# Optimization experiments

Hardware: AMD Instinct MI355X
Metric: run time of the kernel (lower is better)

## Reference

```python
import jax, jax.numpy as jnp
import numpy as np

N = 100000          # number of nodes (nums)
E = 1200000         # nnz of the normalized adjacency
D = 64              # embed_size; layer_size = [64, 64, 64]
NODE_DROP = 0.1     # args.node_dropout[0]
MESS_DROP = (0.1, 0.1, 0.1)
EPS = 1e-12         # F.normalize eps


def setup_inputs() -> dict:
    key = jax.random.key(0)
    ks = jax.random.split(key, 10)
    rows = jax.random.randint(ks[0], (E,), 0, N, dtype=jnp.int32)
    cols = jax.random.randint(ks[1], (E,), 0, N, dtype=jnp.int32)
    vals = jax.random.uniform(ks[2], (E,), dtype=jnp.float32)
    emb = jax.random.normal(ks[3], (N, D), dtype=jnp.float32) * 0.1
    W0 = jax.random.normal(ks[4], (D, D), dtype=jnp.float32) * 0.1
    b0 = jax.random.normal(ks[5], (1, D), dtype=jnp.float32) * 0.1
    W1 = jax.random.normal(ks[6], (D, D), dtype=jnp.float32) * 0.1
    b1 = jax.random.normal(ks[7], (1, D), dtype=jnp.float32) * 0.1
    W2 = jax.random.normal(ks[8], (D, D), dtype=jnp.float32) * 0.1
    b2 = jax.random.normal(ks[9], (1, D), dtype=jnp.float32) * 0.1
    return dict(rows=rows, cols=cols, vals=vals, emb=emb,
                W0=W0, b0=b0, W1=W1, b1=b1, W2=W2, b2=b2)


def reference(rows, cols, vals, emb, W0, b0, W1, b1, W2, b2):
    drop_key = jax.random.key(42)
    k_node, k0, k1, k2 = jax.random.split(drop_key, 4)

    # sparse node dropout: zero dropped edge values (== removing nnz), scale survivors
    keep_e = jax.random.bernoulli(k_node, 1.0 - NODE_DROP, (E,))
    a_vals = jnp.where(keep_e, vals / (1.0 - NODE_DROP), 0.0)

    def layer(ego, W, b, rate, k):
        # SpMM: out[r] += a_vals * ego[c]   (COO scatter-add)
        side = jax.ops.segment_sum(a_vals[:, None] * ego[cols], rows, num_segments=N)
        h = side @ W + b
        keep = jax.random.bernoulli(k, 1.0 - rate, h.shape)
        h = jnp.where(keep, h / (1.0 - rate), 0.0)          # mess dropout
        nrm = h / jnp.maximum(jnp.linalg.norm(h, axis=1, keepdims=True), EPS)
        return h, nrm  # ego continues as the (un-normalized) dropped output

    all_embs = [emb]
    ego = emb
    for (W, b, rate, k) in ((W0, b0, MESS_DROP[0], k0),
                            (W1, b1, MESS_DROP[1], k1),
                            (W2, b2, MESS_DROP[2], k2)):
        ego, nrm = layer(ego, W, b, rate, k)
        all_embs.append(nrm)
    return jnp.concatenate(all_embs, axis=1)  # [N, 4*D]
```

## Files before the change

kernel.cpp:

```cpp
#include <hip/hip_runtime.h>
#include <stdint.h>

#define N_NODES 100000
#define DIM 64
#define E_EDGES 1200000
#define NBK 6250
#define NREP 8
#define BCAP_R 64
#define ROW_CAP 40
#define BPB 16

__host__ __device__ __forceinline__ void tf2x32(uint32_t k0, uint32_t k1,
                                                uint32_t c0, uint32_t c1,
                                                uint32_t& o0, uint32_t& o1) {
    uint32_t ks2 = k0 ^ k1 ^ 0x1BD11BDAu;
    uint32_t x0 = c0 + k0, x1 = c1 + k1;
#define TF_RND(r) { x0 += x1; x1 = (x1 << r) | (x1 >> (32 - r)); x1 ^= x0; }
    TF_RND(13) TF_RND(15) TF_RND(26) TF_RND(6)
    x0 += k1;  x1 += ks2 + 1u;
    TF_RND(17) TF_RND(29) TF_RND(16) TF_RND(24)
    x0 += ks2; x1 += k0 + 2u;
    TF_RND(13) TF_RND(15) TF_RND(26) TF_RND(6)
    x0 += k0;  x1 += k1 + 3u;
    TF_RND(17) TF_RND(29) TF_RND(16) TF_RND(24)
    x0 += k1;  x1 += ks2 + 4u;
    TF_RND(13) TF_RND(15) TF_RND(26) TF_RND(6)
    x0 += ks2; x1 += k0 + 5u;
#undef TF_RND
    o0 = x0; o1 = x1;
}

__device__ __forceinline__ bool keep_bit(uint32_t k0, uint32_t k1, uint32_t idx) {
    uint32_t y0, y1;
    tf2x32(k0, k1, 0u, idx, y0, y1);
    return (((y0 ^ y1) >> 9) < 7549747u);
}

__device__ __forceinline__ uint16_t f2bf(float f) {
    uint32_t x = __float_as_uint(f);
    return (uint16_t)((x + 0x7fffu + ((x >> 16) & 1u)) >> 16);
}

__global__ void k_embcvt(const float* __restrict__ emb, float* __restrict__ out,
                         uint16_t* __restrict__ egoA, int* __restrict__ bcnt) {
    int gid = blockIdx.x * blockDim.x + threadIdx.x;
    if (gid < NREP * NBK) bcnt[gid] = 0;
    int stride = gridDim.x * blockDim.x;
    const int total = N_NODES * 16;
    for (int i = gid; i < total; i += stride) {
        int n = i >> 4, q = i & 15;
        float4 v = ((const float4*)emb)[(size_t)n * 16 + q];
        ((float4*)out)[(size_t)n * 64 + q] = v;
        ushort4 bb;
        bb.x = f2bf(v.x); bb.y = f2bf(v.y); bb.z = f2bf(v.z); bb.w = f2bf(v.w);
        ((ushort4*)egoA)[(size_t)n * 16 + q] = bb;
    }
}

__global__ void k_bucket(const int* __restrict__ rows, const int* __restrict__ cols,
                         const float* __restrict__ vals, int* __restrict__ bcnt,
                         int2* __restrict__ bedge, uint32_t k0, uint32_t k1) {
    int rep = blockIdx.x & (NREP - 1);
    int i = blockIdx.x * blockDim.x + threadIdx.x;
    int stride = gridDim.x * blockDim.x;
    for (; i < E_EDGES; i += stride) {
        if (keep_bit(k0, k1, (uint32_t)i)) {
            int r = rows[i];
            int b = r >> 4;
            int rl = r & 15;
            int cell = rep * NBK + b;
            int pos = atomicAdd(&bcnt[cell], 1);
            if (pos < BCAP_R)
                bedge[(size_t)cell * BCAP_R + pos] =
                    make_int2((rl << 17) | cols[i],
                              __float_as_int(vals[i] * (1.0f / 0.9f)));
        }
    }
}

__global__ __launch_bounds__(256) void k_bin(const int2* __restrict__ bedge,
                                             const int* __restrict__ bcnt,
                                             uint32_t* __restrict__ pairs,
                                             int* __restrict__ cnt) {
    __shared__ uint32_t lp[256 * ROW_CAP];
    __shared__ int lc[256];
    __shared__ int lcc[BPB * NREP];
    int blk = blockIdx.x, t = threadIdx.x;
    for (int i = t; i < 256 * ROW_CAP / 4; i += 256)
        ((uint4*)lp)[i] = make_uint4(0u, 0u, 0u, 0u);
    lc[t] = 0;
    int b0 = blk * BPB;
    if (t < BPB * NREP) {
        int lb = t >> 3, rep = t & 7;
        int ne = bcnt[rep * NBK + b0 + lb];
        lcc[t] = (ne > BCAP_R) ? BCAP_R : ne;
    }
    __syncthreads();
    int e = t & 63, wv = t >> 6;
    for (int cc = 0; cc < BPB * NREP; cc += 4) {
        int cell = cc + wv;
        int lb = cell >> 3, rep = cell & 7;
        int ne = lcc[cell];
        if (e < ne) {
            int2 en = bedge[((size_t)(rep * NBK + b0 + lb)) * BCAP_R + e];
            uint32_t meta = (uint32_t)en.x;
            int rl = (int)(meta >> 17);
            uint32_t col = meta & 0x1FFFFu;
            float v = __int_as_float(en.y);
            int rloc = lb * 16 + rl;
            int pos = atomicAdd(&lc[rloc], 1);
            if (pos < ROW_CAP) {
                uint32_t q = (uint32_t)(v * 16384.0f + 0.5f);
                lp[rloc * ROW_CAP + pos] = (q << 17) | col;
            }
        }
    }
    __syncthreads();
    int nrows = N_NODES - blk * 256;
    if (nrows > 256) nrows = 256;
    int nq = nrows * ROW_CAP / 4;
    uint4* dst = (uint4*)(pairs + (size_t)blk * 256 * ROW_CAP);
    const uint4* src = (const uint4*)lp;
    for (int i = t; i < nq; i += 256) dst[i] = src[i];
    if (t < nrows) cnt[blk * 256 + t] = lc[t];
}

#define GATHER_FMA(V, aE, aO)                                              \
    {                                                                      \
        uint32_t c0 = V.x & 0x1FFFFu;  float a0 = (float)(V.x >> 17) * S;  \
        uint32_t c1 = V.y & 0x1FFFFu;  float a1 = (float)(V.y >> 17) * S;  \
        uint32_t c2 = V.z & 0x1FFFFu;  float a2 = (float)(V.z >> 17) * S;  \
        uint32_t c3 = V.w & 0x1FFFFu;  float a3 = (float)(V.w >> 17) * S;  \
        uint32_t u0 = egoU[c0 * 32u + (uint32_t)l2];                       \
        uint32_t u1 = egoU[c1 * 32u + (uint32_t)l2];                       \
        uint32_t u2 = egoU[c2 * 32u + (uint32_t)l2];                       \
        uint32_t u3 = egoU[c3 * 32u + (uint32_t)l2];                       \
        aE = fmaf(a0, __uint_as_float(u0 << 16), aE);                      \
        aO = fmaf(a0, __uint_as_float(u0 & 0xffff0000u), aO);              \
        aE = fmaf(a1, __uint_as_float(u1 << 16), aE);                      \
        aO = fmaf(a1, __uint_as_float(u1 & 0xffff0000u), aO);              \
        aE = fmaf(a2, __uint_as_float(u2 << 16), aE);                      \
        aO = fmaf(a2, __uint_as_float(u2 & 0xffff0000u), aO);              \
        aE = fmaf(a3, __uint_as_float(u3 << 16), aE);                      \
        aO = fmaf(a3, __uint_as_float(u3 & 0xffff0000u), aO);              \
    }

__global__ __launch_bounds__(256, 4) void k_layer(
    const int* __restrict__ cnt, const uint32_t* __restrict__ pairs,
    const uint16_t* __restrict__ ego_in,
    uint16_t* __restrict__ h_out,
    float* __restrict__ out, int coloff,
    const float* __restrict__ W, const float* __restrict__ bias,
    uint32_t k0, uint32_t k1) {
    __shared__ float sS[8][64];
    int t = threadIdx.x;
    int w = t >> 6, lane = t & 63;

    float wreg[64];
#pragma unroll
    for (int k = 0; k < 64; ++k)
        wreg[k] = W[k * 64 + lane];
    float breg = bias[lane];

    const float S = 1.0f / 16384.0f;
    int l2 = lane & 31;
    int hi4 = (lane >> 5) << 2;
    const uint32_t* egoU = (const uint32_t*)ego_in;
    int wid0 = blockIdx.x * 4 + w;
    const int NW = 2048 * 4;
    const int NPAIR = N_NODES / 2;
    for (int nn = wid0; nn < NPAIR; nn += NW) {
        int un0 = __builtin_amdgcn_readfirstlane(nn * 2);
        int un1 = un0 + 1;
        int len0 = (cnt[un0] + 7) & ~7;  if (len0 > ROW_CAP) len0 = ROW_CAP;
        int len1 = (cnt[un1] + 7) & ~7;  if (len1 > ROW_CAP) len1 = ROW_CAP;
        const uint32_t* rowp0 = pairs + (size_t)un0 * ROW_CAP + hi4;
        const uint32_t* rowp1 = pairs + (size_t)un1 * ROW_CAP + hi4;
        float accE0 = 0.f, accO0 = 0.f, accE1 = 0.f, accO1 = 0.f;
        int jmax = len0 > len1 ? len0 : len1;
        for (int j = 0; j < jmax; j += 8) {
            uint4 V0 = (j < len0) ? *reinterpret_cast<const uint4*>(rowp0 + j)
                                  : make_uint4(0u, 0u, 0u, 0u);
            uint4 V1 = (j < len1) ? *reinterpret_cast<const uint4*>(rowp1 + j)
                                  : make_uint4(0u, 0u, 0u, 0u);
            GATHER_FMA(V0, accE0, accO0)
            GATHER_FMA(V1, accE1, accO1)
        }
        accE0 += __shfl_xor(accE0, 32, 64);
        accO0 += __shfl_xor(accO0, 32, 64);
        accE1 += __shfl_xor(accE1, 32, 64);
        accO1 += __shfl_xor(accO1, 32, 64);
        if (lane < 32) {
            reinterpret_cast<float2*>(&sS[2 * w][0])[l2] = make_float2(accE0, accO0);
            reinterpret_cast<float2*>(&sS[2 * w + 1][0])[l2] = make_float2(accE1, accO1);
        }
        float h0 = breg, h1 = breg;
        const float4* s4p0 = reinterpret_cast<const float4*>(&sS[2 * w][0]);
        const float4* s4p1 = reinterpret_cast<const float4*>(&sS[2 * w + 1][0]);
#pragma unroll
        for (int kq = 0; kq < 16; ++kq) {
            float4 s40 = s4p0[kq];
            float4 s41 = s4p1[kq];
            h0 = fmaf(s40.x, wreg[4 * kq + 0], h0);
            h1 = fmaf(s41.x, wreg[4 * kq + 0], h1);
            h0 = fmaf(s40.y, wreg[4 * kq + 1], h0);
            h1 = fmaf(s41.y, wreg[4 * kq + 1], h1);
            h0 = fmaf(s40.z, wreg[4 * kq + 2], h0);
            h1 = fmaf(s41.z, wreg[4 * kq + 2], h1);
            h0 = fmaf(s40.w, wreg[4 * kq + 3], h0);
            h1 = fmaf(s41.w, wreg[4 * kq + 3], h1);
        }
        h0 = keep_bit(k0, k1, (uint32_t)un0 * 64u + (uint32_t)lane) ? h0 * (1.0f / 0.9f) : 0.0f;
        h1 = keep_bit(k0, k1, (uint32_t)un1 * 64u + (uint32_t)lane) ? h1 * (1.0f / 0.9f) : 0.0f;
        float s0 = h0 * h0, s1 = h1 * h1;
#pragma unroll
        for (int o = 32; o > 0; o >>= 1) {
            s0 += __shfl_xor(s0, o, 64);
            s1 += __shfl_xor(s1, o, 64);
        }
        float nv0 = h0 / fmaxf(sqrtf(s0), 1e-12f);
        float nv1 = h1 / fmaxf(sqrtf(s1), 1e-12f);
        if (h_out) {
            h_out[(size_t)un0 * DIM + lane] = f2bf(h0);
            h_out[(size_t)un1 * DIM + lane] = f2bf(h1);
        }
        out[(size_t)un0 * 256 + coloff + lane] = nv0;
        out[(size_t)un1 * 256 + coloff + lane] = nv1;
    }
}

extern "C" void kernel_launch(void* const* d_in, const int* in_sizes, int n_in,
                              void* d_out, int out_size, void* d_ws, size_t ws_size,
                              hipStream_t stream) {
    const int*   rows = (const int*)d_in[0];
    const int*   cols = (const int*)d_in[1];
    const float* vals = (const float*)d_in[2];
    const float* emb  = (const float*)d_in[3];
    const float* Wk[3] = { (const float*)d_in[4], (const float*)d_in[6], (const float*)d_in[8] };
    const float* bk[3] = { (const float*)d_in[5], (const float*)d_in[7], (const float*)d_in[9] };
    float* out = (float*)d_out;

    int*      bcnt  = (int*)d_ws;
    int*      cnt   = bcnt + 65536;
    int2*     bedge = (int2*)(cnt + 100000 + 14);
    bedge = (int2*)(((uintptr_t)bedge + 511) & ~(uintptr_t)511);
    uint32_t* pairs = (uint32_t*)(bedge + (size_t)NREP * NBK * BCAP_R);
    uint16_t* egoA  = (uint16_t*)(pairs + (size_t)N_NODES * ROW_CAP);
    uint16_t* egoB  = egoA + (size_t)N_NODES * DIM;

    uint32_t kn[2], kl[3][2];
    tf2x32(0u, 42u, 0u, 0u, kn[0], kn[1]);
    tf2x32(0u, 42u, 0u, 1u, kl[0][0], kl[0][1]);
    tf2x32(0u, 42u, 0u, 2u, kl[1][0], kl[1][1]);
    tf2x32(0u, 42u, 0u, 3u, kl[2][0], kl[2][1]);

    k_embcvt<<<2048, 256, 0, stream>>>(emb, out, egoA, bcnt);
    k_bucket<<<2048, 256, 0, stream>>>(rows, cols, vals, bcnt, bedge, kn[0], kn[1]);
    k_bin<<<(NBK + BPB - 1) / BPB, 256, 0, stream>>>(bedge, bcnt, pairs, cnt);

    k_layer<<<2048, 256, 0, stream>>>(cnt, pairs, egoA, egoB, out, 64,
                                      Wk[0], bk[0], kl[0][0], kl[0][1]);
    k_layer<<<2048, 256, 0, stream>>>(cnt, pairs, egoB, egoA, out, 128,
                                      Wk[1], bk[1], kl[1][0], kl[1][1]);
    k_layer<<<2048, 256, 0, stream>>>(cnt, pairs, egoA, nullptr, out, 192,
                                      Wk[2], bk[2], kl[2][0], kl[2][1]);
}
```

Measured before the change: 231.9 us.

## Precompute dropout masks in bucket kernel and prefetch next row's edge pairs

All three layers' message-dropout keep bits are now generated once in k_bucket, using wave ballots into 64-bit masks, so the layer kernels no longer run Threefry per element. k_layer also software-pipelines the row gather. It prefetches the count and first edge vector of the next node pair, and unconditionally loads the first two vectors of the current pair before the loop. The cost is extra mask storage and reads, some register pressure, and possibly wasted loads of padding entries for short rows.

```diff
diff --git a/kernel.cpp b/kernel.cpp
--- a/kernel.cpp
+++ b/kernel.cpp
@@ -59,7 +59,10 @@
 
 __global__ void k_bucket(const int* __restrict__ rows, const int* __restrict__ cols,
                          const float* __restrict__ vals, int* __restrict__ bcnt,
-                         int2* __restrict__ bedge, uint32_t k0, uint32_t k1) {
+                         int2* __restrict__ bedge, uint64_t* __restrict__ masks,
+                         uint32_t k0, uint32_t k1,
+                         uint32_t ka0, uint32_t ka1, uint32_t kb0, uint32_t kb1,
+                         uint32_t kc0, uint32_t kc1) {
     int rep = blockIdx.x & (NREP - 1);
     int i = blockIdx.x * blockDim.x + threadIdx.x;
     int stride = gridDim.x * blockDim.x;
@@ -74,6 +77,23 @@
                 bedge[(size_t)cell * BCAP_R + pos] =
                     make_int2((rl << 17) | cols[i],
                               __float_as_int(vals[i] * (1.0f / 0.9f)));
+        }
+    }
+    int lane = threadIdx.x & 63;
+    int wv = blockIdx.x * (blockDim.x >> 6) + (threadIdx.x >> 6);
+    const int NMW = (N_NODES + 8191) / 8192;
+    for (int k = 0; k < NMW; ++k) {
+        int n = wv * NMW + k;
+        if (n < N_NODES) {
+            uint32_t idx = (uint32_t)n * 64u + (uint32_t)lane;
+            uint64_t m0 = __ballot(keep_bit(ka0, ka1, idx));
+            uint64_t m1 = __ballot(keep_bit(kb0, kb1, idx));
+            uint64_t m2 = __ballot(keep_bit(kc0, kc1, idx));
+            if (lane == 0) {
+                masks[n] = m0;
+                masks[N_NODES + n] = m1;
+                masks[2 * N_NODES + n] = m2;
+            }
         }
     }
 }
@@ -151,7 +171,7 @@
     uint16_t* __restrict__ h_out,
     float* __restrict__ out, int coloff,
     const float* __restrict__ W, const float* __restrict__ bias,
-    uint32_t k0, uint32_t k1) {
+    const uint64_t* __restrict__ lmask) {
     __shared__ float sS[8][64];
     int t = threadIdx.x;
     int w = t >> 6, lane = t & 63;
@@ -169,20 +189,49 @@
     int wid0 = blockIdx.x * 4 + w;
     const int NW = 2048 * 4;
     const int NPAIR = N_NODES / 2;
+
+    uint4 pA0, pA1;
+    int pl0 = 0, pl1 = 0;
+    if (wid0 < NPAIR) {
+        int u = __builtin_amdgcn_readfirstlane(wid0 * 2);
+        pl0 = cnt[u];
+        pl1 = cnt[u + 1];
+        pA0 = *reinterpret_cast<const uint4*>(pairs + (size_t)u * ROW_CAP + hi4);
+        pA1 = *reinterpret_cast<const uint4*>(pairs + (size_t)(u + 1) * ROW_CAP + hi4);
+    }
+
     for (int nn = wid0; nn < NPAIR; nn += NW) {
         int un0 = __builtin_amdgcn_readfirstlane(nn * 2);
         int un1 = un0 + 1;
-        int len0 = (cnt[un0] + 7) & ~7;  if (len0 > ROW_CAP) len0 = ROW_CAP;
-        int len1 = (cnt[un1] + 7) & ~7;  if (len1 > ROW_CAP) len1 = ROW_CAP;
+        uint4 A0 = pA0, A1 = pA1;
+        int l0 = pl0, l1 = pl1;
         const uint32_t* rowp0 = pairs + (size_t)un0 * ROW_CAP + hi4;
         const uint32_t* rowp1 = pairs + (size_t)un1 * ROW_CAP + hi4;
+        uint4 B0 = *reinterpret_cast<const uint4*>(rowp0 + 8);
+        uint4 B1 = *reinterpret_cast<const uint4*>(rowp1 + 8);
+        int nx = nn + NW;
+        if (nx < NPAIR) {
+            int u = __builtin_amdgcn_readfirstlane(nx * 2);
+            pl0 = cnt[u];
+            pl1 = cnt[u + 1];
+            pA0 = *reinterpret_cast<const uint4*>(pairs + (size_t)u * ROW_CAP + hi4);
+            pA1 = *reinterpret_cast<const uint4*>(pairs + (size_t)(u + 1) * ROW_CAP + hi4);
+        }
+        uint64_t m0 = lmask[un0];
+        uint64_t m1 = lmask[un1];
+
         float accE0 = 0.f, accO0 = 0.f, accE1 = 0.f, accO1 = 0.f;
+        GATHER_FMA(A0, accE0, accO0)
+        GATHER_FMA(A1, accE1, accO1)
+        GATHER_FMA(B0, accE0, accO0)
+        GATHER_FMA(B1, accE1, accO1)
+        int len0 = (l0 + 7) & ~7;  if (len0 > ROW_CAP) len0 = ROW_CAP;
+        int len1 = (l1 + 7) & ~7;  if (len1 > ROW_CAP) len1 = ROW_CAP;
         int jmax = len0 > len1 ? len0 : len1;
-        for (int j = 0; j < jmax; j += 8) {
-            uint4 V0 = (j < len0) ? *reinterpret_cast<const uint4*>(rowp0 + j)
-                                  : make_uint4(0u, 0u, 0u, 0u);
-            uint4 V1 = (j < len1) ? *reinterpret_cast<const uint4*>(rowp1 + j)
-                                  : make_uint4(0u, 0u, 0u, 0u);
+        const uint4 zed = make_uint4(0u, 0u, 0u, 0u);
+        for (int j = 16; j < jmax; j += 8) {
+            uint4 V0 = (j < len0) ? *reinterpret_cast<const uint4*>(rowp0 + j) : zed;
+            uint4 V1 = (j < len1) ? *reinterpret_cast<const uint4*>(rowp1 + j) : zed;
             GATHER_FMA(V0, accE0, accO0)
             GATHER_FMA(V1, accE1, accO1)
         }
@@ -210,8 +259,8 @@
             h0 = fmaf(s40.w, wreg[4 * kq + 3], h0);
             h1 = fmaf(s41.w, wreg[4 * kq + 3], h1);
         }
-        h0 = keep_bit(k0, k1, (uint32_t)un0 * 64u + (uint32_t)lane) ? h0 * (1.0f / 0.9f) : 0.0f;
-        h1 = keep_bit(k0, k1, (uint32_t)un1 * 64u + (uint32_t)lane) ? h1 * (1.0f / 0.9f) : 0.0f;
+        h0 = ((m0 >> lane) & 1ull) ? h0 * (1.0f / 0.9f) : 0.0f;
+        h1 = ((m1 >> lane) & 1ull) ? h1 * (1.0f / 0.9f) : 0.0f;
         float s0 = h0 * h0, s1 = h1 * h1;
 #pragma unroll
         for (int o = 32; o > 0; o >>= 1) {
@@ -242,7 +291,9 @@
 
     int*      bcnt  = (int*)d_ws;
     int*      cnt   = bcnt + 65536;
-    int2*     bedge = (int2*)(cnt + 100000 + 14);
+    uint64_t* masks = (uint64_t*)((char*)d_ws + 262144 + 400000 + 1696);
+    masks = (uint64_t*)(((uintptr_t)masks + 511) & ~(uintptr_t)511);
+    int2*     bedge = (int2*)(masks + 3 * N_NODES);
     bedge = (int2*)(((uintptr_t)bedge + 511) & ~(uintptr_t)511);
     uint32_t* pairs = (uint32_t*)(bedge + (size_t)NREP * NBK * BCAP_R);
     uint16_t* egoA  = (uint16_t*)(pairs + (size_t)N_NODES * ROW_CAP);
@@ -255,13 +306,16 @@
     tf2x32(0u, 42u, 0u, 3u, kl[2][0], kl[2][1]);
 
     k_embcvt<<<2048, 256, 0, stream>>>(emb, out, egoA, bcnt);
-    k_bucket<<<2048, 256, 0, stream>>>(rows, cols, vals, bcnt, bedge, kn[0], kn[1]);
+    k_bucket<<<2048, 256, 0, stream>>>(rows, cols, vals, bcnt, bedge, masks,
+                                       kn[0], kn[1],
+                                       kl[0][0], kl[0][1], kl[1][0], kl[1][1],
+                                       kl[2][0], kl[2][1]);
     k_bin<<<(NBK + BPB - 1) / BPB, 256, 0, stream>>>(bedge, bcnt, pairs, cnt);
 
     k_layer<<<2048, 256, 0, stream>>>(cnt, pairs, egoA, egoB, out, 64,
-                                      Wk[0], bk[0], kl[0][0], kl[0][1]);
+                                      Wk[0], bk[0], masks);
     k_layer<<<2048, 256, 0, stream>>>(cnt, pairs, egoB, egoA, out, 128,
-                                      Wk[1], bk[1], kl[1][0], kl[1][1]);
+                                      Wk[1], bk[1], masks + N_NODES);
     k_layer<<<2048, 256, 0, stream>>>(cnt, pairs, egoA, nullptr, out, 192,
-                                      Wk[2], bk[2], kl[2][0], kl[2][1]);
-}
+                                      Wk[2], bk[2], masks + 2 * N_NODES);
+}
```

Measured after the change: 312.2 us. +34.6%, slower.

## Pack bucketed edges into 32-bit words and fuse embedding conversion into bucketing

Applied to the files above, without the earlier changes.

Bucketed edge records shrink from int2 (col plus float value) to a single 32-bit word holding the 4-bit local row, an 11-bit quantized value and a 17-bit column. This halves bucket write and read traffic between k_bucket and k_bin. The embedding copy and bf16 conversion now run inside k_bucket after the edge loop, and a small k_zero kernel takes over clearing the counters. The value quantization drops from 14 bits to 11 bits, so edge weights lose precision, which risks accuracy error in the SpMM.

```diff
diff --git a/kernel.cpp b/kernel.cpp
--- a/kernel.cpp
+++ b/kernel.cpp
@@ -41,11 +41,35 @@
     return (uint16_t)((x + 0x7fffu + ((x >> 16) & 1u)) >> 16);
 }
 
-__global__ void k_embcvt(const float* __restrict__ emb, float* __restrict__ out,
-                         uint16_t* __restrict__ egoA, int* __restrict__ bcnt) {
+__global__ void k_zero(int* __restrict__ bcnt) {
     int gid = blockIdx.x * blockDim.x + threadIdx.x;
-    if (gid < NREP * NBK) bcnt[gid] = 0;
     int stride = gridDim.x * blockDim.x;
+    for (int i = gid; i < NREP * NBK; i += stride) bcnt[i] = 0;
+}
+
+__global__ void k_bucket(const int* __restrict__ rows, const int* __restrict__ cols,
+                         const float* __restrict__ vals,
+                         const float* __restrict__ emb, float* __restrict__ out,
+                         uint16_t* __restrict__ egoA,
+                         int* __restrict__ bcnt, uint32_t* __restrict__ bedge,
+                         uint32_t k0, uint32_t k1) {
+    int rep = blockIdx.x & (NREP - 1);
+    int gid = blockIdx.x * blockDim.x + threadIdx.x;
+    int stride = gridDim.x * blockDim.x;
+    for (int i = gid; i < E_EDGES; i += stride) {
+        if (keep_bit(k0, k1, (uint32_t)i)) {
+            int r = rows[i];
+            int b = r >> 4;
+            int rl = r & 15;
+            int cell = rep * NBK + b;
+            int pos = atomicAdd(&bcnt[cell], 1);
+            if (pos < BCAP_R) {
+                uint32_t q = (uint32_t)(vals[i] * (1024.0f / 0.9f) + 0.5f);
+                bedge[(size_t)cell * BCAP_R + pos] =
+                    ((uint32_t)rl << 28) | (q << 17) | (uint32_t)cols[i];
+            }
+        }
+    }
     const int total = N_NODES * 16;
     for (int i = gid; i < total; i += stride) {
         int n = i >> 4, q = i & 15;
@@ -57,28 +81,7 @@
     }
 }
 
-__global__ void k_bucket(const int* __restrict__ rows, const int* __restrict__ cols,
-                         const float* __restrict__ vals, int* __restrict__ bcnt,
-                         int2* __restrict__ bedge, uint32_t k0, uint32_t k1) {
-    int rep = blockIdx.x & (NREP - 1);
-    int i = blockIdx.x * blockDim.x + threadIdx.x;
-    int stride = gridDim.x * blockDim.x;
-    for (; i < E_EDGES; i += stride) {
-        if (keep_bit(k0, k1, (uint32_t)i)) {
-            int r = rows[i];
-            int b = r >> 4;
-            int rl = r & 15;
-            int cell = rep * NBK + b;
-            int pos = atomicAdd(&bcnt[cell], 1);
-            if (pos < BCAP_R)
-                bedge[(size_t)cell * BCAP_R + pos] =
-                    make_int2((rl << 17) | cols[i],
-                              __float_as_int(vals[i] * (1.0f / 0.9f)));
-        }
-    }
-}
-
-__global__ __launch_bounds__(256) void k_bin(const int2* __restrict__ bedge,
+__global__ __launch_bounds__(256) void k_bin(const uint32_t* __restrict__ bedge,
                                              const int* __restrict__ bcnt,
                                              uint32_t* __restrict__ pairs,
                                              int* __restrict__ cnt) {
@@ -102,17 +105,14 @@
         int lb = cell >> 3, rep = cell & 7;
         int ne = lcc[cell];
         if (e < ne) {
-            int2 en = bedge[((size_t)(rep * NBK + b0 + lb)) * BCAP_R + e];
-            uint32_t meta = (uint32_t)en.x;
-            int rl = (int)(meta >> 17);
-            uint32_t col = meta & 0x1FFFFu;
-            float v = __int_as_float(en.y);
+            uint32_t en = bedge[((size_t)(rep * NBK + b0 + lb)) * BCAP_R + e];
+            int rl = (int)(en >> 28);
+            uint32_t q11 = (en >> 17) & 0x7FFu;
+            uint32_t col = en & 0x1FFFFu;
             int rloc = lb * 16 + rl;
             int pos = atomicAdd(&lc[rloc], 1);
-            if (pos < ROW_CAP) {
-                uint32_t q = (uint32_t)(v * 16384.0f + 0.5f);
-                lp[rloc * ROW_CAP + pos] = (q << 17) | col;
-            }
+            if (pos < ROW_CAP)
+                lp[rloc * ROW_CAP + pos] = (q11 << 21) | col;
         }
     }
     __syncthreads();
@@ -242,9 +242,9 @@
 
     int*      bcnt  = (int*)d_ws;
     int*      cnt   = bcnt + 65536;
-    int2*     bedge = (int2*)(cnt + 100000 + 14);
-    bedge = (int2*)(((uintptr_t)bedge + 511) & ~(uintptr_t)511);
-    uint32_t* pairs = (uint32_t*)(bedge + (size_t)NREP * NBK * BCAP_R);
+    uint32_t* bedge = (uint32_t*)(cnt + 100000 + 14);
+    bedge = (uint32_t*)(((uintptr_t)bedge + 511) & ~(uintptr_t)511);
+    uint32_t* pairs = bedge + (size_t)NREP * NBK * BCAP_R;
     uint16_t* egoA  = (uint16_t*)(pairs + (size_t)N_NODES * ROW_CAP);
     uint16_t* egoB  = egoA + (size_t)N_NODES * DIM;
 
@@ -254,8 +254,9 @@
     tf2x32(0u, 42u, 0u, 2u, kl[1][0], kl[1][1]);
     tf2x32(0u, 42u, 0u, 3u, kl[2][0], kl[2][1]);
 
-    k_embcvt<<<2048, 256, 0, stream>>>(emb, out, egoA, bcnt);
-    k_bucket<<<2048, 256, 0, stream>>>(rows, cols, vals, bcnt, bedge, kn[0], kn[1]);
+    k_zero<<<64, 256, 0, stream>>>(bcnt);
+    k_bucket<<<2048, 256, 0, stream>>>(rows, cols, vals, emb, out, egoA,
+                                       bcnt, bedge, kn[0], kn[1]);
     k_bin<<<(NBK + BPB - 1) / BPB, 256, 0, stream>>>(bedge, bcnt, pairs, cnt);
 
     k_layer<<<2048, 256, 0, stream>>>(cnt, pairs, egoA, egoB, out, 64,
```

New measurement: 230.3 us. Within noise of the previous version (-0.7%).
